# Kernel optimization log

Measured on AMD Instinct MI355X. Metric: run time of the kernel, lower is better.

## Reference

```python
import jax, jax.numpy as jnp
import numpy as np

EMB = 1024
HEADS = 16
HEAD_DIM = EMB // HEADS

def setup_inputs() -> dict:
    key = jax.random.key(0)
    ks = jax.random.split(key, 12)
    s = 0.02
    x = jax.random.normal(ks[0], (2, 2048, EMB), dtype=jnp.float32)
    return {
        "x": x,
        "wq": jax.random.normal(ks[1], (EMB, EMB), jnp.float32) * s,
        "bq": jnp.zeros((EMB,), jnp.float32),
        "wk": jax.random.normal(ks[2], (EMB, EMB), jnp.float32) * s,
        "bk": jnp.zeros((EMB,), jnp.float32),
        "wv": jax.random.normal(ks[3], (EMB, EMB), jnp.float32) * s,
        "bv": jnp.zeros((EMB,), jnp.float32),
        "wo": jax.random.normal(ks[4], (EMB, EMB), jnp.float32) * s,
        "bo": jnp.zeros((EMB,), jnp.float32),
        "gamma": jnp.ones((EMB,), jnp.float32),
        "beta": jnp.zeros((EMB,), jnp.float32),
    }

def _layernorm(x, gamma, beta, eps=1e-5):
    mu = jnp.mean(x, axis=-1, keepdims=True)
    var = jnp.mean(jnp.square(x - mu), axis=-1, keepdims=True)
    return (x - mu) * jax.lax.rsqrt(var + eps) * gamma + beta

def reference(x, wq, bq, wk, bk, wv, bv, wo, bo, gamma, beta):
    B, T, D = x.shape
    H, d_k = HEADS, HEAD_DIM
    # Linear(y = x W^T + b), then split heads
    q = (x @ wq.T + bq).reshape(B, T, H, d_k)
    k = (x @ wk.T + bk).reshape(B, T, H, d_k)
    v = (x @ wv.T + bv).reshape(B, T, H, d_k)
    scores = jnp.einsum('bthd,bshd->bhts', q, k) / jnp.sqrt(jnp.float32(d_k))
    attn = jax.nn.softmax(scores, axis=-1)  # dropout is identity in eval mode
    out = jnp.einsum('bhts,bshd->bthd', attn, v).reshape(B, T, D)
    out = out @ wo.T + bo
    return _layernorm(x + out, gamma, beta)
```

## Files before the change

kernel.cpp:

```cpp
#include <hip/hip_runtime.h>
#include <stdint.h>
#include <stddef.h>


typedef __bf16 bf16_t;
typedef bf16_t bf16x8 __attribute__((ext_vector_type(8)));
typedef float f32x16 __attribute__((ext_vector_type(16)));
typedef uint16_t u16x8 __attribute__((ext_vector_type(8)));

#define MFMA32(a, b, c) __builtin_amdgcn_mfma_f32_32x32x16_bf16((a), (b), (c), 0, 0, 0)

__device__ __forceinline__ uint16_t f2bf(float f) {
  __bf16 h = (__bf16)f;
  return *(uint16_t*)&h;
}

__device__ __forceinline__ void gload16(const void* g, void* l) {
  __builtin_amdgcn_global_load_lds((const __attribute__((address_space(1))) void*)g,
                                   (__attribute__((address_space(3))) void*)l,
                                   16, 0, 0);
}

__global__ __launch_bounds__(256) void cvt_all(
    const float* __restrict__ x, const float* __restrict__ wq,
    const float* __restrict__ wk, const float* __restrict__ wv,
    const float* __restrict__ wo, uint16_t* __restrict__ xb,
    uint16_t* __restrict__ wqb, uint16_t* __restrict__ wkb,
    uint16_t* __restrict__ wvb, uint16_t* __restrict__ wob) {
  const int gid = blockIdx.x * 256 + threadIdx.x;
  const float* src; uint16_t* dst; int off;
  if (gid < 1048576) {
    src = x; dst = xb; off = gid;
  } else {
    const int t = gid - 1048576;
    off = t & 262143;
    switch (t >> 18) {
      case 0: src = wq; dst = wqb; break;
      case 1: src = wk; dst = wkb; break;
      case 2: src = wv; dst = wvb; break;
      default: src = wo; dst = wob; break;
    }
  }
  const float4 f = ((const float4*)src)[off];
  uint64_t p = (uint64_t)f2bf(f.x) | ((uint64_t)f2bf(f.y) << 16) |
               ((uint64_t)f2bf(f.z) << 32) | ((uint64_t)f2bf(f.w) << 48);
  ((uint64_t*)dst)[off] = p;
}

template <bool OUT_BF16>
__device__ __forceinline__ void gemm128(const uint16_t* __restrict__ A,
                                        const uint16_t* __restrict__ Bt,
                                        const float* __restrict__ bias,
                                        float oscale,
                                        uint16_t* __restrict__ outb,
                                        float* __restrict__ outf) {
  __shared__ uint16_t sA[2][128 * 32];
  __shared__ uint16_t sB[2][128 * 32];
  const int tid = threadIdx.x;
  const int lane = tid & 63, w = tid >> 6;
  const int l31 = lane & 31, half = lane >> 5;
  const int m0 = blockIdx.y * 128, n0 = blockIdx.x * 128;
  const int wm = (w >> 1) * 64, wn = (w & 1) * 64;

  const int ch0 = tid, ch1 = tid + 256;
  const int r0 = ch0 >> 2, g0 = (((ch0 & 3) ^ (r0 & 3)) << 3);
  const int r1 = ch1 >> 2, g1 = (((ch1 & 3) ^ (r1 & 3)) << 3);
  const uint16_t* a0 = A + (size_t)(m0 + r0) * 1024 + g0;
  const uint16_t* a1 = A + (size_t)(m0 + r1) * 1024 + g1;
  const uint16_t* b0 = Bt + (size_t)(n0 + r0) * 1024 + g0;
  const uint16_t* b1 = Bt + (size_t)(n0 + r1) * 1024 + g1;

  gload16(a0, &sA[0][ch0 * 8]);
  gload16(a1, &sA[0][ch1 * 8]);
  gload16(b0, &sB[0][ch0 * 8]);
  gload16(b1, &sB[0][ch1 * 8]);

  f32x16 acc[2][2] = {};

  for (int kt = 0; kt < 32; ++kt) {
    __syncthreads();
    const int cur = kt & 1;
    if (kt < 31) {
      const int ko = (kt + 1) * 32;
      const int nxt = cur ^ 1;
      gload16(a0 + ko, &sA[nxt][ch0 * 8]);
      gload16(a1 + ko, &sA[nxt][ch1 * 8]);
      gload16(b0 + ko, &sB[nxt][ch0 * 8]);
      gload16(b1 + ko, &sB[nxt][ch1 * 8]);
    }
#pragma unroll
    for (int s = 0; s < 2; ++s) {
      const int c = s * 2 + half;
      bf16x8 af[2], bfr[2];
#pragma unroll
      for (int i = 0; i < 2; ++i) {
        const int arow = wm + i * 32 + l31;
        af[i] = *(const bf16x8*)&sA[cur][arow * 32 + ((c ^ (arow & 3)) << 3)];
      }
#pragma unroll
      for (int j = 0; j < 2; ++j) {
        const int brow = wn + j * 32 + l31;
        bfr[j] = *(const bf16x8*)&sB[cur][brow * 32 + ((c ^ (brow & 3)) << 3)];
      }
#pragma unroll
      for (int i = 0; i < 2; ++i)
#pragma unroll
        for (int j = 0; j < 2; ++j) acc[i][j] = MFMA32(af[i], bfr[j], acc[i][j]);
    }
  }

#pragma unroll
  for (int i = 0; i < 2; ++i) {
#pragma unroll
    for (int j = 0; j < 2; ++j) {
      const int gn = n0 + wn + j * 32 + l31;
      const float bv = bias[gn];
#pragma unroll
      for (int reg = 0; reg < 16; ++reg) {
        const int gm = m0 + wm + i * 32 + (reg & 3) + 8 * (reg >> 2) + 4 * half;
        const float v = (acc[i][j][reg] + bv) * oscale;
        const size_t idx = (size_t)gm * 1024 + gn;
        if constexpr (OUT_BF16) outb[idx] = f2bf(v);
        else outf[idx] = v;
      }
    }
  }
}

#define QSCALE 0.18033688011112042f

__global__ __launch_bounds__(256) void qkv_gemm(
    const uint16_t* __restrict__ xb, const uint16_t* __restrict__ wqb,
    const uint16_t* __restrict__ wkb, const uint16_t* __restrict__ wvb,
    const float* __restrict__ bq, const float* __restrict__ bk,
    const float* __restrict__ bv, uint16_t* __restrict__ qb,
    uint16_t* __restrict__ kb, uint16_t* __restrict__ vb) {
  const uint16_t* Bt; const float* bias; uint16_t* out; float sc;
  if (blockIdx.z == 0)      { Bt = wqb; bias = bq; out = qb; sc = QSCALE; }
  else if (blockIdx.z == 1) { Bt = wkb; bias = bk; out = kb; sc = 1.f; }
  else                      { Bt = wvb; bias = bv; out = vb; sc = 1.f; }
  gemm128<true>(xb, Bt, bias, sc, out, nullptr);
}

__global__ __launch_bounds__(256) void o_gemm(const uint16_t* __restrict__ ab,
                                              const uint16_t* __restrict__ wob,
                                              const float* __restrict__ bo,
                                              float* __restrict__ y) {
  gemm128<false>(ab, wob, bo, 1.f, nullptr, y);
}

__global__ __launch_bounds__(256) void v_trans(const uint16_t* __restrict__ vb,
                                               uint16_t* __restrict__ vbT) {
  __shared__ uint16_t sT[64 * 136];
  const int tid = threadIdx.x;
  const int t0 = blockIdx.x * 128;
  const int h = blockIdx.y, b = blockIdx.z;
#pragma unroll
  for (int c = 0; c < 4; ++c) {
    const int idx = c * 256 + tid;
    const int t = idx >> 3, d8 = (idx & 7) * 8;
    u16x8 v = *(const u16x8*)&vb[(size_t)(b * 2048 + t0 + t) * 1024 + h * 64 + d8];
#pragma unroll
    for (int e = 0; e < 8; ++e) sT[(d8 + e) * 136 + t] = v[e];
  }
  __syncthreads();
  const size_t obase = ((size_t)(b * 16 + h) * 64) * 2048 + t0;
#pragma unroll
  for (int c = 0; c < 4; ++c) {
    const int idx = c * 256 + tid;
    const int d = idx >> 4, t8 = (idx & 15) * 8;
    u16x8 v = *(const u16x8*)&sT[d * 136 + t8];
    *(u16x8*)&vbT[obase + (size_t)d * 2048 + t8] = v;
  }
}

__global__ __launch_bounds__(512, 4) void attn(const uint16_t* __restrict__ qb,
                                               const uint16_t* __restrict__ kb,
                                               const uint16_t* __restrict__ vbT,
                                               uint16_t* __restrict__ ab) {
  __shared__ __align__(16) uint16_t smem[40960];
  uint16_t* sK = smem;
  uint16_t* sV = smem + 16384;
  uint16_t* sP = smem + 32768;
  const int tid = threadIdx.x;
  const int lane = tid & 63, w = tid >> 6;
  const int l31 = lane & 31, half = lane >> 5;
  const int rg = w & 3, sh = w >> 2;
  const int hb = blockIdx.x;
  const int h = hb & 15, b = hb >> 4;
  const int q0 = blockIdx.y * 128;
  const size_t qkbase = (size_t)b * 2048 * 1024 + (size_t)h * 64;
  const size_t vtbase = (size_t)hb * 64 * 2048;

  const int ch0 = tid, ch1 = tid + 512;
  const int kr0 = ch0 >> 3, kg0 = (((ch0 & 7) ^ (kr0 & 7)) << 3);
  const int kr1 = ch1 >> 3, kg1 = (((ch1 & 7) ^ (kr1 & 7)) << 3);
  const int vr0 = ch0 >> 4, vg0 = (((ch0 & 15) ^ (vr0 & 15)) << 3);
  const int vr1 = ch1 >> 4, vg1 = (((ch1 & 15) ^ (vr1 & 15)) << 3);
  const uint16_t* k0 = kb + qkbase + (size_t)kr0 * 1024 + kg0;
  const uint16_t* k1 = kb + qkbase + (size_t)kr1 * 1024 + kg1;
  const uint16_t* v0 = vbT + vtbase + (size_t)vr0 * 2048 + vg0;
  const uint16_t* v1 = vbT + vtbase + (size_t)vr1 * 2048 + vg1;

  gload16(k0, sK + ch0 * 8);
  gload16(k1, sK + ch1 * 8);
  gload16(v0, sV + ch0 * 8);
  gload16(v1, sV + ch1 * 8);

  bf16x8 qa[4];
  {
    const uint16_t* qrow =
        qb + qkbase + (size_t)(q0 + rg * 32 + l31) * 1024 + half * 8;
#pragma unroll
    for (int s4 = 0; s4 < 4; ++s4) qa[s4] = *(const bf16x8*)(qrow + s4 * 16);
  }

  f32x16 acc_o[2] = {};
  float li[16];
#pragma unroll
  for (int r = 0; r < 16; ++r) li[r] = 0.f;

  uint16_t* sPw = sP + w * 1024;
  __bf16* sPb = (__bf16*)sPw;

  for (int kt = 0; kt < 16; ++kt) {
    __syncthreads();
    const int cur = kt & 1;
    if (kt < 15) {
      const size_t soK = (size_t)(kt + 1) * 128 * 1024;
      const int soV = (kt + 1) * 128;
      const int nxt = cur ^ 1;
      gload16(k0 + soK, sK + nxt * 8192 + ch0 * 8);
      gload16(k1 + soK, sK + nxt * 8192 + ch1 * 8);
      gload16(v0 + soV, sV + nxt * 8192 + ch0 * 8);
      gload16(v1 + soV, sV + nxt * 8192 + ch1 * 8);
    }
    const uint16_t* sKc = sK + cur * 8192;
    const uint16_t* sVc = sV + cur * 8192;

    f32x16 acc_s[2] = {};
#pragma unroll
    for (int s4 = 0; s4 < 4; ++s4) {
      const int c = s4 * 2 + half;
#pragma unroll
      for (int n = 0; n < 2; ++n) {
        const int brow = sh * 64 + n * 32 + l31;
        const bf16x8 kk =
            *(const bf16x8*)&sKc[brow * 64 + ((c ^ (brow & 7)) << 3)];
        acc_s[n] = MFMA32(qa[s4], kk, acc_s[n]);
      }
    }

#pragma unroll
    for (int n = 0; n < 2; ++n) {
#pragma unroll
      for (int reg = 0; reg < 16; ++reg) {
        const float p = __builtin_amdgcn_exp2f(acc_s[n][reg]);
        li[reg] += p;
        const int row = (reg & 3) + 8 * (reg >> 2) + 4 * half;
        sPb[row * 32 + (((l31 >> 3) ^ (row & 3)) << 3) + (l31 & 7)] = (__bf16)p;
      }
#pragma unroll
      for (int st = 0; st < 2; ++st) {
        const int c2 = st * 2 + half;
        const bf16x8 pa = *(const bf16x8*)&sPw[l31 * 32 + ((c2 ^ (l31 & 3)) << 3)];
#pragma unroll
        for (int n2 = 0; n2 < 2; ++n2) {
          const int vrow = n2 * 32 + l31;
          const int c3 = sh * 8 + n * 4 + st * 2 + half;
          const bf16x8 vv =
              *(const bf16x8*)&sVc[vrow * 128 + ((c3 ^ (vrow & 15)) << 3)];
          acc_o[n2] = MFMA32(pa, vv, acc_o[n2]);
        }
      }
    }
  }

  __syncthreads();
  float* ep = (float*)smem;
  float* epl = (float*)(smem + 16384);
  if (sh == 1) {
#pragma unroll
    for (int n2 = 0; n2 < 2; ++n2)
#pragma unroll
      for (int reg = 0; reg < 16; ++reg)
        ep[((rg * 2 + n2) * 16 + reg) * 64 + lane] = acc_o[n2][reg];
#pragma unroll
    for (int reg = 0; reg < 16; ++reg)
      epl[(rg * 16 + reg) * 64 + lane] = li[reg];
  }
  __syncthreads();
  if (sh == 0) {
#pragma unroll
    for (int n2 = 0; n2 < 2; ++n2)
#pragma unroll
      for (int reg = 0; reg < 16; ++reg)
        acc_o[n2][reg] += ep[((rg * 2 + n2) * 16 + reg) * 64 + lane];
#pragma unroll
    for (int reg = 0; reg < 16; ++reg) {
      float s = li[reg] + epl[(rg * 16 + reg) * 64 + lane];
#pragma unroll
      for (int o = 1; o < 32; o <<= 1) s += __shfl_xor(s, o);
      li[reg] = 1.f / s;
    }
#pragma unroll
    for (int n2 = 0; n2 < 2; ++n2)
#pragma unroll
      for (int reg = 0; reg < 16; ++reg) {
        const int row = q0 + rg * 32 + (reg & 3) + 8 * (reg >> 2) + 4 * half;
        const int col = h * 64 + n2 * 32 + l31;
        ab[(size_t)(b * 2048 + row) * 1024 + col] =
            f2bf(acc_o[n2][reg] * li[reg]);
      }
  }
}

__global__ __launch_bounds__(256) void resid_ln(const float* __restrict__ x,
                                                const float* __restrict__ y,
                                                const float* __restrict__ gamma,
                                                const float* __restrict__ beta,
                                                float* __restrict__ out) {
  const int row = blockIdx.x, tid = threadIdx.x;
  const size_t base = (size_t)row * 1024 + tid * 4;
  const float4 xv = *(const float4*)(x + base);
  const float4 yv = *(const float4*)(y + base);
  const float a = xv.x + yv.x, b2 = xv.y + yv.y, c = xv.z + yv.z, d = xv.w + yv.w;
  float s = a + b2 + c + d;
#pragma unroll
  for (int o = 1; o < 64; o <<= 1) s += __shfl_xor(s, o);
  __shared__ float red[4];
  const int w = tid >> 6;
  if ((tid & 63) == 0) red[w] = s;
  __syncthreads();
  const float mu = (red[0] + red[1] + red[2] + red[3]) * (1.f / 1024.f);
  const float da = a - mu, db = b2 - mu, dc = c - mu, dd = d - mu;
  float sq = da * da + db * db + dc * dc + dd * dd;
#pragma unroll
  for (int o = 1; o < 64; o <<= 1) sq += __shfl_xor(sq, o);
  __syncthreads();
  if ((tid & 63) == 0) red[w] = sq;
  __syncthreads();
  const float var = (red[0] + red[1] + red[2] + red[3]) * (1.f / 1024.f);
  const float rs = rsqrtf(var + 1e-5f);
  const float4 g = *(const float4*)(gamma + tid * 4);
  const float4 bt = *(const float4*)(beta + tid * 4);
  float4 o4;
  o4.x = da * rs * g.x + bt.x;
  o4.y = db * rs * g.y + bt.y;
  o4.z = dc * rs * g.z + bt.z;
  o4.w = dd * rs * g.w + bt.w;
  *(float4*)(out + base) = o4;
}

extern "C" void kernel_launch(void* const* d_in, const int* in_sizes, int n_in,
                              void* d_out, int out_size, void* d_ws, size_t ws_size,
                              hipStream_t stream) {
  const float* x     = (const float*)d_in[0];
  const float* wq    = (const float*)d_in[1];
  const float* bq    = (const float*)d_in[2];
  const float* wk    = (const float*)d_in[3];
  const float* bk    = (const float*)d_in[4];
  const float* wv    = (const float*)d_in[5];
  const float* bv    = (const float*)d_in[6];
  const float* wo    = (const float*)d_in[7];
  const float* bo    = (const float*)d_in[8];
  const float* gamma = (const float*)d_in[9];
  const float* beta  = (const float*)d_in[10];
  float* out = (float*)d_out;
  char* ws = (char*)d_ws;
  const size_t MB = 1024 * 1024;
  uint16_t* xb  = (uint16_t*)(ws);
  uint16_t* ab  = xb;
  uint16_t* wqb = (uint16_t*)(ws + 8 * MB);
  uint16_t* wkb = (uint16_t*)(ws + 10 * MB);
  uint16_t* wvb = (uint16_t*)(ws + 12 * MB);
  uint16_t* wob = (uint16_t*)(ws + 14 * MB);
  uint16_t* qb  = (uint16_t*)(ws + 16 * MB);
  uint16_t* kb  = (uint16_t*)(ws + 24 * MB);
  uint16_t* vb  = (uint16_t*)(ws + 32 * MB);
  uint16_t* vbT = (uint16_t*)(ws + 40 * MB);
  float*    y   = (float*)(ws + 16 * MB);

  cvt_all<<<8192, 256, 0, stream>>>(x, wq, wk, wv, wo, xb, wqb, wkb, wvb, wob);
  qkv_gemm<<<dim3(8, 32, 3), 256, 0, stream>>>(xb, wqb, wkb, wvb, bq, bk, bv, qb, kb, vb);
  v_trans<<<dim3(16, 16, 2), 256, 0, stream>>>(vb, vbT);
  attn<<<dim3(32, 16), 512, 0, stream>>>(qb, kb, vbT, ab);
  o_gemm<<<dim3(8, 32), 256, 0, stream>>>(ab, wob, bo, y);
  resid_ln<<<4096, 256, 0, stream>>>(x, y, gamma, beta, out);
}
```

Before: 227.0 us.

## Compute transposed S=K·Q^T so P feeds PV MFMA directly from registers

The attention kernel now computes the score tile transposed (K as the A operand, Q as B), so each lane's exp'd probabilities can be packed straight into the B operand of the P·V MFMA. This drops the per-wave shared-memory round trip for P, the sP buffer, and the per-row shuffle reduction of the softmax denominator, which becomes one scalar per lane. To match the new MFMA operand layout, the V transpose kernel permutes elements within each group of 16, and the output is written as packed 64-bit stores. LDS use per block also shrinks.

```diff
diff --git a/kernel.cpp b/kernel.cpp
--- a/kernel.cpp
+++ b/kernel.cpp
@@ -169,7 +169,12 @@
   for (int c = 0; c < 4; ++c) {
     const int idx = c * 256 + tid;
     const int d = idx >> 4, t8 = (idx & 15) * 8;
-    u16x8 v = *(const u16x8*)&sT[d * 136 + t8];
+    const int tb = t8 & ~15;
+    const int add4 = (t8 & 8) ? 4 : 0;
+    u16x8 v;
+#pragma unroll
+    for (int e = 0; e < 8; ++e)
+      v[e] = sT[d * 136 + tb + ((e & 3) + ((e >> 2) << 3)) + add4];
     *(u16x8*)&vbT[obase + (size_t)d * 2048 + t8] = v;
   }
 }
@@ -178,10 +183,9 @@
                                                const uint16_t* __restrict__ kb,
                                                const uint16_t* __restrict__ vbT,
                                                uint16_t* __restrict__ ab) {
-  __shared__ __align__(16) uint16_t smem[40960];
+  __shared__ __align__(16) uint16_t smem[32768];
   uint16_t* sK = smem;
   uint16_t* sV = smem + 16384;
-  uint16_t* sP = smem + 32768;
   const int tid = threadIdx.x;
   const int lane = tid & 63, w = tid >> 6;
   const int l31 = lane & 31, half = lane >> 5;
@@ -216,12 +220,7 @@
   }
 
   f32x16 acc_o[2] = {};
-  float li[16];
-#pragma unroll
-  for (int r = 0; r < 16; ++r) li[r] = 0.f;
-
-  uint16_t* sPw = sP + w * 1024;
-  __bf16* sPb = (__bf16*)sPw;
+  float li = 0.f;
 
   for (int kt = 0; kt < 16; ++kt) {
     __syncthreads();
@@ -238,39 +237,40 @@
     const uint16_t* sKc = sK + cur * 8192;
     const uint16_t* sVc = sV + cur * 8192;
 
-    f32x16 acc_s[2] = {};
-#pragma unroll
-    for (int s4 = 0; s4 < 4; ++s4) {
-      const int c = s4 * 2 + half;
-#pragma unroll
-      for (int n = 0; n < 2; ++n) {
-        const int brow = sh * 64 + n * 32 + l31;
+#pragma unroll
+    for (int mblk = 0; mblk < 2; ++mblk) {
+      f32x16 accs = {};
+#pragma unroll
+      for (int s4 = 0; s4 < 4; ++s4) {
+        const int c = s4 * 2 + half;
+        const int srow = sh * 64 + mblk * 32 + l31;
         const bf16x8 kk =
-            *(const bf16x8*)&sKc[brow * 64 + ((c ^ (brow & 7)) << 3)];
-        acc_s[n] = MFMA32(qa[s4], kk, acc_s[n]);
-      }
-    }
-
-#pragma unroll
-    for (int n = 0; n < 2; ++n) {
-#pragma unroll
-      for (int reg = 0; reg < 16; ++reg) {
-        const float p = __builtin_amdgcn_exp2f(acc_s[n][reg]);
-        li[reg] += p;
-        const int row = (reg & 3) + 8 * (reg >> 2) + 4 * half;
-        sPb[row * 32 + (((l31 >> 3) ^ (row & 3)) << 3) + (l31 & 7)] = (__bf16)p;
-      }
-#pragma unroll
-      for (int st = 0; st < 2; ++st) {
-        const int c2 = st * 2 + half;
-        const bf16x8 pa = *(const bf16x8*)&sPw[l31 * 32 + ((c2 ^ (l31 & 3)) << 3)];
-#pragma unroll
-        for (int n2 = 0; n2 < 2; ++n2) {
-          const int vrow = n2 * 32 + l31;
-          const int c3 = sh * 8 + n * 4 + st * 2 + half;
+            *(const bf16x8*)&sKc[srow * 64 + ((c ^ (srow & 7)) << 3)];
+        accs = MFMA32(kk, qa[s4], accs);
+      }
+      bf16x8 bp0, bp1;
+#pragma unroll
+      for (int reg = 0; reg < 8; ++reg) {
+        const float p = __builtin_amdgcn_exp2f(accs[reg]);
+        li += p;
+        bp0[reg] = (__bf16)p;
+      }
+#pragma unroll
+      for (int reg = 8; reg < 16; ++reg) {
+        const float p = __builtin_amdgcn_exp2f(accs[reg]);
+        li += p;
+        bp1[reg - 8] = (__bf16)p;
+      }
+#pragma unroll
+      for (int t = 0; t < 2; ++t) {
+        const bf16x8 bp = t ? bp1 : bp0;
+        const int cc = sh * 8 + mblk * 4 + t * 2 + half;
+#pragma unroll
+        for (int md = 0; md < 2; ++md) {
+          const int vrow = md * 32 + l31;
           const bf16x8 vv =
-              *(const bf16x8*)&sVc[vrow * 128 + ((c3 ^ (vrow & 15)) << 3)];
-          acc_o[n2] = MFMA32(pa, vv, acc_o[n2]);
+              *(const bf16x8*)&sVc[vrow * 128 + ((cc ^ (vrow & 15)) << 3)];
+          acc_o[md] = MFMA32(vv, bp, acc_o[md]);
         }
       }
     }
@@ -281,36 +281,33 @@
   float* epl = (float*)(smem + 16384);
   if (sh == 1) {
 #pragma unroll
-    for (int n2 = 0; n2 < 2; ++n2)
+    for (int md = 0; md < 2; ++md)
 #pragma unroll
       for (int reg = 0; reg < 16; ++reg)
-        ep[((rg * 2 + n2) * 16 + reg) * 64 + lane] = acc_o[n2][reg];
-#pragma unroll
-    for (int reg = 0; reg < 16; ++reg)
-      epl[(rg * 16 + reg) * 64 + lane] = li[reg];
+        ep[((rg * 2 + md) * 16 + reg) * 64 + lane] = acc_o[md][reg];
+    epl[rg * 64 + lane] = li;
   }
   __syncthreads();
   if (sh == 0) {
 #pragma unroll
-    for (int n2 = 0; n2 < 2; ++n2)
+    for (int md = 0; md < 2; ++md)
 #pragma unroll
       for (int reg = 0; reg < 16; ++reg)
-        acc_o[n2][reg] += ep[((rg * 2 + n2) * 16 + reg) * 64 + lane];
-#pragma unroll
-    for (int reg = 0; reg < 16; ++reg) {
-      float s = li[reg] + epl[(rg * 16 + reg) * 64 + lane];
-#pragma unroll
-      for (int o = 1; o < 32; o <<= 1) s += __shfl_xor(s, o);
-      li[reg] = 1.f / s;
-    }
-#pragma unroll
-    for (int n2 = 0; n2 < 2; ++n2)
-#pragma unroll
-      for (int reg = 0; reg < 16; ++reg) {
-        const int row = q0 + rg * 32 + (reg & 3) + 8 * (reg >> 2) + 4 * half;
-        const int col = h * 64 + n2 * 32 + l31;
-        ab[(size_t)(b * 2048 + row) * 1024 + col] =
-            f2bf(acc_o[n2][reg] * li[reg]);
+        acc_o[md][reg] += ep[((rg * 2 + md) * 16 + reg) * 64 + lane];
+    li += epl[rg * 64 + lane];
+    li += __shfl_xor(li, 32);
+    const float inv = 1.f / li;
+    const int row = q0 + rg * 32 + l31;
+    uint16_t* const obase = ab + (size_t)(b * 2048 + row) * 1024 + h * 64;
+#pragma unroll
+    for (int md = 0; md < 2; ++md)
+#pragma unroll
+      for (int g = 0; g < 4; ++g) {
+        uint64_t pk = 0;
+#pragma unroll
+        for (int e = 0; e < 4; ++e)
+          pk |= (uint64_t)f2bf(acc_o[md][g * 4 + e] * inv) << (16 * e);
+        *(uint64_t*)(obase + md * 32 + g * 8 + half * 4) = pk;
       }
   }
 }
```

After: 207.9 us. 8.4% less time.
